# Performance work log

Measured on AMD Instinct MI355X. Metric: run time of the kernel, lower is better.

The kernel has to match this reference:

```python
import jax, jax.numpy as jnp
import numpy as np

B, L, D_IN, D_MODEL, D_OUT, N_LAYERS, N2 = 16, 2048, 512, 512, 512, 4, 32
Q_STEP = 1.0 / 64.0
LN_EPS = 1e-5


def setup_inputs() -> dict:
    key = jax.random.key(0)
    ks = jax.random.split(key, 12)
    H = D_MODEL
    x = jax.random.normal(ks[0], (B, D_IN, L), jnp.float32)
    # sigma-delta dense encoder / decoder weights (ANN-equivalent: dense + ReLU)
    W_enc = jax.random.normal(ks[1], (H, D_IN), jnp.float32) * (1.0 / np.sqrt(D_IN))
    W_dec = jax.random.normal(ks[2], (D_OUT, H), jnp.float32) * (1.0 / np.sqrt(H))
    # S4D kernel params, stacked over layers. S4D-Lin init.
    log_dt = (jax.random.uniform(ks[3], (N_LAYERS, H), jnp.float32)
              * (np.log(0.1) - np.log(0.001)) + np.log(0.001))
    log_A_real = jnp.full((N_LAYERS, H, N2), np.log(0.5), jnp.float32)
    A_imag = jnp.tile((np.pi * jnp.arange(N2, dtype=jnp.float32))[None, None, :],
                      (N_LAYERS, H, 1))
    C_re = jax.random.normal(ks[4], (N_LAYERS, H, N2), jnp.float32) * (0.5 ** 0.5)
    C_im = jax.random.normal(ks[5], (N_LAYERS, H, N2), jnp.float32) * (0.5 ** 0.5)
    D = jax.random.normal(ks[6], (N_LAYERS, H), jnp.float32)
    # output linear of each S4D block: 1x1 conv H -> 2H followed by GLU
    W_out = jax.random.normal(ks[7], (N_LAYERS, 2 * H, H), jnp.float32) * (1.0 / np.sqrt(H))
    b_out = jnp.zeros((N_LAYERS, 2 * H), jnp.float32)
    ln_g = jnp.ones((N_LAYERS, H), jnp.float32)
    ln_b = jnp.zeros((N_LAYERS, H), jnp.float32)
    return {"x": x, "W_enc": W_enc, "W_dec": W_dec, "log_dt": log_dt,
            "log_A_real": log_A_real, "A_imag": A_imag, "C_re": C_re,
            "C_im": C_im, "D": D, "W_out": W_out, "b_out": b_out,
            "ln_g": ln_g, "ln_b": ln_b}


def _quantize_ste(x, step):
    q = jnp.round(x / step) * step
    return x + jax.lax.stop_gradient(q - x)


def reference(x, W_enc, W_dec, log_dt, log_A_real, A_imag, C_re, C_im, D,
              W_out, b_out, ln_g, ln_b):
    # x: (B, d_input, L) channel-time layout (slayer convention)
    xq = _quantize_ste(x, Q_STEP)
    h = jax.nn.relu(jnp.einsum('bct,dc->bdt', xq, W_enc))  # encoder (B,H,L)
    Lx = h.shape[-1]
    t = jnp.arange(Lx)
    for i in range(N_LAYERS):
        # ---- S4D kernel (ZOH-style discretization) ----
        dt = jnp.exp(log_dt[i])[:, None]                 # (H,1)
        A = -jnp.exp(log_A_real[i]) + 1j * A_imag[i]     # (H,N)
        dtA = dt * A                                     # (H,N)
        Cc = (C_re[i] + 1j * C_im[i]) * jnp.expm1(dtA) / A
        vand = jnp.exp(dtA[:, :, None] * t)              # (H,N,L)
        K = 2.0 * jnp.einsum('hn,hnl->hl', Cc, vand).real  # (H,L)
        # ---- FFT convolution ----
        k_f = jnp.fft.rfft(K, n=2 * Lx)                  # (H, L+1)
        u_f = jnp.fft.rfft(h, n=2 * Lx)                  # (B,H,L+1)
        y = jnp.fft.irfft(u_f * k_f[None], n=2 * Lx)[..., :Lx]
        y = y + D[i][:, None] * h                        # skip connection
        y = jax.nn.gelu(y, approximate=False)
        # output linear: 1x1 conv H->2H + GLU over channel dim
        z = jnp.einsum('bht,dh->bdt', y, W_out[i]) + b_out[i][None, :, None]
        z = z[:, :D_MODEL] * jax.nn.sigmoid(z[:, D_MODEL:])
        # residual + post-norm (LayerNorm over channel dim)
        h = z + h
        mu = h.mean(axis=1, keepdims=True)
        var = h.var(axis=1, keepdims=True)
        h = (h - mu) / jnp.sqrt(var + LN_EPS) * ln_g[i][:, None] + ln_b[i][:, None]
    out = jax.nn.relu(jnp.einsum('bht,dh->bdt', h, W_dec))  # decoder (B,d_out,L)
    return out
```

## Files before the change

### kernel.cpp

```cpp
#include <hip/hip_runtime.h>
#include <cstdint>
#include <cstddef>

typedef __attribute__((ext_vector_type(8))) short short8;
typedef __attribute__((ext_vector_type(8))) _Float16 half8;
typedef __attribute__((ext_vector_type(4))) float floatx4;
typedef __attribute__((ext_vector_type(4))) int intx4;
typedef __attribute__((ext_vector_type(4))) unsigned short ushort4v;

__device__ __forceinline__ unsigned short f2h(float f) {
    union { _Float16 h; unsigned short u; } v;
    v.h = (_Float16)f;
    return v.u;
}
__device__ __forceinline__ float h2f(unsigned short u) {
    union { unsigned short u; _Float16 h; } v;
    v.u = u;
    return (float)v.h;
}
__device__ __forceinline__ float relu_keepnan(float v) {
    return v > 0.f ? v : (v == v ? 0.f : v);
}

__global__ __launch_bounds__(256) void k_cvt(
    const float* __restrict__ src, unsigned short* __restrict__ dst, int n) {
    int i = blockIdx.x * 256 + threadIdx.x;
    if (i < n) dst[i] = f2h(src[i]);
}

__global__ __launch_bounds__(256) void k_precompute(
    const float* __restrict__ ldt, const float* __restrict__ lar,
    const float* __restrict__ aim, const float* __restrict__ cre,
    const float* __restrict__ cim, float4* __restrict__ lwc,
    float2* __restrict__ wt) {
    int idx = blockIdx.x * 256 + threadIdx.x;
    int i = idx >> 14;
    int h = (idx >> 5) & 511;
    int n = idx & 31;
    float dt = expf(ldt[i * 512 + h]);
    float Are = -expf(lar[idx]);
    float Aim = aim[idx];
    float dre = dt * Are, dim = dt * Aim;
    float e = expf(dre);
    float wre = e * cosf(dim);
    float wim = e * sinf(dim);
    float emr = wre - 1.f, emi = wim;
    float inv = 1.f / (Are * Are + Aim * Aim);
    float fr = (emr * Are + emi * Aim) * inv;
    float fi = (emi * Are - emr * Aim) * inv;
    float cr = cre[idx], ci = cim[idx];
    float4 o;
    o.x = wre; o.y = wim;
    o.z = 2.f * (cr * fr - ci * fi);
    o.w = 2.f * (cr * fi + ci * fr);
    int oidx = (i * 32 + n) * 512 + h;
    lwc[oidx] = o;
    float ar = wre, ai = wim;
#pragma unroll
    for (int k = 0; k < 7; ++k) {
        float nr = ar * ar - ai * ai;
        float ni = 2.f * ar * ai;
        ar = nr; ai = ni;
    }
    wt[oidx] = make_float2(ar, ai);
}

__global__ __launch_bounds__(256) void k_quant_transpose(
    const float* __restrict__ x, unsigned short* __restrict__ xq, int b0) {
    __shared__ unsigned short tile[64][65];
    const int bg = b0 + blockIdx.z, bl = blockIdx.z;
    const int c0 = blockIdx.y * 64, t0 = blockIdx.x * 64;
    const int tid = threadIdx.x;
#pragma unroll
    for (int it = 0; it < 16; ++it) {
        int idx = it * 256 + tid;
        int r = idx >> 6, cc = idx & 63;
        float f = x[(size_t)(bg * 512 + c0 + r) * 2048 + t0 + cc];
        float q = rintf(f * 64.f) * 0.015625f;
        tile[r][cc] = f2h(q);
    }
    __syncthreads();
#pragma unroll
    for (int it = 0; it < 16; ++it) {
        int idx = it * 256 + tid;
        int r = idx >> 6, cc = idx & 63;
        xq[(size_t)(bl * 2048 + t0 + r) * 512 + c0 + cc] = tile[cc][r];
    }
}

__global__ __launch_bounds__(64) void k_build_wa(
    const float4* __restrict__ lwc, unsigned short* __restrict__ WA, int layer) {
    __shared__ unsigned short Ws[64 * 136];
    const int h = blockIdx.x, tid = threadIdx.x;
    if (tid < 32) {
        float4 v = lwc[((size_t)layer * 32 + tid) * 512 + h];
        float pr = 1.f, pi = 0.f;
        for (int m = 0; m < 128; ++m) {
            Ws[(2 * tid) * 136 + (127 - m)] = f2h(pr);
            Ws[(2 * tid + 1) * 136 + (127 - m)] = f2h(pi);
            float nr = pr * v.x - pi * v.y;
            float ni = pr * v.y + pi * v.x;
            pr = nr; pi = ni;
        }
    }
    __syncthreads();
#pragma unroll
    for (int it = 0; it < 16; ++it) {
        int idx = it * 64 + tid;
        int r = idx >> 4, c8 = idx & 15;
        *(intx4*)(WA + (size_t)h * 8192 + r * 128 + c8 * 8) =
            *(const intx4*)(Ws + r * 136 + c8 * 8);
    }
}

__global__ __launch_bounds__(256) void k_build_T(
    const float4* __restrict__ lwc, const float* __restrict__ Dp,
    unsigned short* __restrict__ TT, int layer) {
    __shared__ float Kvs[128];
    __shared__ unsigned short Mxs[128 * 64];
    __shared__ float wr_s[32], wi_s[32], cr_s[32], ci_s[32];
    const int h = blockIdx.x, tid = threadIdx.x;
    if (tid < 32) {
        float4 v = lwc[((size_t)layer * 32 + tid) * 512 + h];
        wr_s[tid] = v.x; wi_s[tid] = v.y; cr_s[tid] = v.z; ci_s[tid] = v.w;
    }
    __syncthreads();
    if (tid < 32) {
        const int n = tid;
        float wre = wr_s[n], wim = wi_s[n];
        float ar = cr_s[n], ai = ci_s[n];
        for (int m = 0; m <= 128; ++m) {
            if (m < 128) {
                float s = ar;
#pragma unroll
                for (int d = 16; d >= 1; d >>= 1) s += __shfl_xor(s, d, 64);
                if (n == 0) Kvs[m] = s;
            }
            if (m >= 1) {
                Mxs[(m - 1) * 64 + 2 * n] = f2h(ar);
                Mxs[(m - 1) * 64 + 2 * n + 1] = f2h(-ai);
            }
            float nr = ar * wre - ai * wim;
            float ni = ar * wim + ai * wre;
            ar = nr; ai = ni;
        }
    }
    __syncthreads();
    const float Dh = Dp[layer * 512 + h];
#pragma unroll
    for (int it = 0; it < 12; ++it) {
        int idx = it * 256 + tid;
        int t = idx / 24, c8 = idx % 24;
        short8 pack;
#pragma unroll
        for (int q = 0; q < 8; ++q) {
            int k = c8 * 8 + q;
            unsigned short us;
            if (k < 128) {
                float val = (k <= t) ? (Kvs[t - k] + (k == t ? Dh : 0.f)) : 0.f;
                us = f2h(val);
            } else {
                us = Mxs[t * 64 + (k - 128)];
            }
            pack[q] = (short)us;
        }
        *(short8*)(TT + (size_t)h * 24576 + t * 192 + c8 * 8) = pack;
    }
}

template <int MODE>
__global__ __launch_bounds__(256, 2) void k_gemm(
    const unsigned short* __restrict__ A, const unsigned short* __restrict__ Bm,
    float* __restrict__ of32, unsigned short* __restrict__ o16,
    unsigned short* __restrict__ ut, int J, int b0) {
    __shared__ __align__(16) unsigned short lds[2 * 128 * 72];
    unsigned short* Al = lds;
    unsigned short* Bl = lds + 128 * 72;
    const int tid = threadIdx.x;
    const int m0 = blockIdx.y * 128;
    const int j0 = blockIdx.x * 128;
    const int sub = tid & 7;
    const int row = tid >> 3;
    const unsigned short* Ag = A + (size_t)(m0 + row) * 512 + sub * 8;
    const unsigned short* Bg = Bm + (size_t)(j0 + row) * 512 + sub * 8;
    intx4 ra[4], rb[4];
#pragma unroll
    for (int i = 0; i < 4; ++i) {
        ra[i] = *(const intx4*)(Ag + (size_t)i * 32 * 512);
        rb[i] = *(const intx4*)(Bg + (size_t)i * 32 * 512);
    }
    const int lane = tid & 63;
    const int w = tid >> 6;
    const int wm = w & 1, wn = w >> 1;
    const int l15 = lane & 15, quad = lane >> 4;
    floatx4 acc[4][4] = {};
    for (int kt = 0; kt < 8; ++kt) {
#pragma unroll
        for (int i = 0; i < 4; ++i) {
            *(intx4*)(Al + (row + 32 * i) * 72 + sub * 8) = ra[i];
            *(intx4*)(Bl + (row + 32 * i) * 72 + sub * 8) = rb[i];
        }
        __syncthreads();
        if (kt < 7) {
#pragma unroll
            for (int i = 0; i < 4; ++i) {
                ra[i] = *(const intx4*)(Ag + (size_t)i * 32 * 512 + (kt + 1) * 64);
                rb[i] = *(const intx4*)(Bg + (size_t)i * 32 * 512 + (kt + 1) * 64);
            }
        }
#pragma unroll
        for (int ks = 0; ks < 2; ++ks) {
            half8 af[4], bfr[4];
#pragma unroll
            for (int mt = 0; mt < 4; ++mt)
                af[mt] = *(const half8*)(Al + (wm * 64 + mt * 16 + l15) * 72 + ks * 32 + quad * 8);
#pragma unroll
            for (int nt = 0; nt < 4; ++nt)
                bfr[nt] = *(const half8*)(Bl + (wn * 64 + nt * 16 + l15) * 72 + ks * 32 + quad * 8);
#pragma unroll
            for (int mt = 0; mt < 4; ++mt)
#pragma unroll
                for (int nt = 0; nt < 4; ++nt)
                    acc[mt][nt] = __builtin_amdgcn_mfma_f32_16x16x32_f16(
                        af[mt], bfr[nt], acc[mt][nt], 0, 0, 0);
        }
        __syncthreads();
    }
#pragma unroll
    for (int mt = 0; mt < 4; ++mt) {
#pragma unroll
        for (int nt = 0; nt < 4; ++nt) {
            const int dl = wm * 64 + mt * 16 + quad * 4;
            const int jl = wn * 64 + nt * 16 + l15;
            floatx4 v = acc[mt][nt];
#pragma unroll
            for (int r = 0; r < 4; ++r) v[r] = relu_keepnan(v[r]);
            if (MODE == 0) {
                ushort4v hv;
#pragma unroll
                for (int r = 0; r < 4; ++r) hv[r] = f2h(v[r]);
                *(ushort4v*)(o16 + (size_t)(j0 + jl) * 512 + m0 + dl) = hv;
#pragma unroll
                for (int r = 0; r < 4; ++r) lds[(dl + r) * 136 + jl] = hv[r];
            } else {
                const int j = j0 + jl;
                const int bl = j >> 11, t = j & 2047;
#pragma unroll
                for (int r = 0; r < 4; ++r)
                    of32[((size_t)((b0 + bl) * 512 + m0 + dl + r)) * 2048 + t] = v[r];
            }
        }
    }
    if (MODE == 0) {
        __syncthreads();
        const int drow = tid >> 1, hh = tid & 1;
        const unsigned short* srcp = lds + drow * 136 + hh * 64;
        unsigned short* dstp = ut + (size_t)(m0 + drow) * J + j0 + hh * 64;
#pragma unroll
        for (int q = 0; q < 8; ++q)
            *(intx4*)(dstp + q * 8) = *(const intx4*)(srcp + q * 8);
    }
}

__global__ __launch_bounds__(256, 4) void k_stateA(
    const unsigned short* __restrict__ WA, const unsigned short* __restrict__ ut,
    float* __restrict__ P, int J, int Rtot) {
    __shared__ __align__(16) unsigned short Aw[64 * 72];
    __shared__ __align__(16) unsigned short Bw[128 * 72];
    const int tid = threadIdx.x;
    const int h = blockIdx.y;
    const int r0 = blockIdx.x * 128;
    const int sub = tid & 7, row = tid >> 3;
    const unsigned short* Ag = WA + (size_t)h * 8192 + row * 128 + sub * 8;
    const unsigned short* Bg = ut + (size_t)h * J + (size_t)(r0 + row) * 128 + sub * 8;
    intx4 ra[2], rb[4];
    ra[0] = *(const intx4*)(Ag);
    ra[1] = *(const intx4*)(Ag + 32 * 128);
#pragma unroll
    for (int i = 0; i < 4; ++i) rb[i] = *(const intx4*)(Bg + i * 32 * 128);
    const int lane = tid & 63, w = tid >> 6;
    const int wm = w & 1, wn = w >> 1;
    const int l15 = lane & 15, quad = lane >> 4;
    floatx4 acc[2][4] = {};
    for (int kt = 0; kt < 2; ++kt) {
        *(intx4*)(Aw + row * 72 + sub * 8) = ra[0];
        *(intx4*)(Aw + (row + 32) * 72 + sub * 8) = ra[1];
#pragma unroll
        for (int i = 0; i < 4; ++i)
            *(intx4*)(Bw + (row + 32 * i) * 72 + sub * 8) = rb[i];
        __syncthreads();
        if (kt == 0) {
            ra[0] = *(const intx4*)(Ag + 64);
            ra[1] = *(const intx4*)(Ag + 32 * 128 + 64);
#pragma unroll
            for (int i = 0; i < 4; ++i) rb[i] = *(const intx4*)(Bg + i * 32 * 128 + 64);
        }
#pragma unroll
        for (int ks = 0; ks < 2; ++ks) {
            half8 af[2], bfr[4];
#pragma unroll
            for (int mt = 0; mt < 2; ++mt)
                af[mt] = *(const half8*)(Aw + (wm * 32 + mt * 16 + l15) * 72 + ks * 32 + quad * 8);
#pragma unroll
            for (int nt = 0; nt < 4; ++nt)
                bfr[nt] = *(const half8*)(Bw + (wn * 64 + nt * 16 + l15) * 72 + ks * 32 + quad * 8);
#pragma unroll
            for (int mt = 0; mt < 2; ++mt)
#pragma unroll
                for (int nt = 0; nt < 4; ++nt)
                    acc[mt][nt] = __builtin_amdgcn_mfma_f32_16x16x32_f16(
                        af[mt], bfr[nt], acc[mt][nt], 0, 0, 0);
        }
        __syncthreads();
    }
#pragma unroll
    for (int mt = 0; mt < 2; ++mt)
#pragma unroll
        for (int nt = 0; nt < 4; ++nt)
#pragma unroll
            for (int r = 0; r < 4; ++r)
                P[((size_t)h * 64 + wm * 32 + mt * 16 + quad * 4 + r) * Rtot +
                  r0 + wn * 64 + nt * 16 + l15] = acc[mt][nt][r];
}

__global__ __launch_bounds__(64) void k_comb(
    const float* __restrict__ P, const float2* __restrict__ wt,
    unsigned short* __restrict__ S0, int layer, int Rtot) {
    __shared__ float Ps[64][17];
    __shared__ unsigned short S0s[16][64];
    const int h = blockIdx.x, bl = blockIdx.y;
    const int tid = threadIdx.x;
#pragma unroll
    for (int it = 0; it < 4; ++it) {
        int idx = it * 64 + tid;
        int n2 = idx >> 2, pt = idx & 3;
        float4 v = *(const float4*)(P + ((size_t)h * 64 + n2) * Rtot + bl * 16 + pt * 4);
        Ps[n2][pt * 4 + 0] = v.x; Ps[n2][pt * 4 + 1] = v.y;
        Ps[n2][pt * 4 + 2] = v.z; Ps[n2][pt * 4 + 3] = v.w;
    }
    __syncthreads();
    if (tid < 32) {
        const int n = tid;
        float2 wv = wt[((size_t)layer * 32 + n) * 512 + h];
        float ar = 0.f, ai = 0.f;
        for (int g = 0; g < 16; ++g) {
            S0s[g][2 * n] = f2h(ar);
            S0s[g][2 * n + 1] = f2h(ai);
            float pr = Ps[2 * n][g], pi = Ps[2 * n + 1][g];
            float nr = fmaf(wv.x, ar, fmaf(-wv.y, ai, pr));
            float ni = fmaf(wv.x, ai, fmaf(wv.y, ar, pi));
            ar = nr; ai = ni;
        }
    }
    __syncthreads();
    const int g = tid >> 2, pt = tid & 3;
    unsigned short* dst = S0 + ((size_t)h * Rtot + bl * 16 + g) * 64 + pt * 16;
    *(intx4*)(dst) = *(const intx4*)(&S0s[g][pt * 16]);
    *(intx4*)(dst + 8) = *(const intx4*)(&S0s[g][pt * 16 + 8]);
}

__global__ __launch_bounds__(256, 2) void k_applyB(
    const unsigned short* __restrict__ TT, const unsigned short* __restrict__ ut,
    const unsigned short* __restrict__ S0, unsigned short* __restrict__ vt,
    int J, int Rtot) {
    __shared__ __align__(16) unsigned short lds[2 * 128 * 72];
    unsigned short* Al = lds;
    unsigned short* Bl = lds + 128 * 72;
    const int tid = threadIdx.x;
    const int h = blockIdx.y;
    const int r0 = blockIdx.x * 128;
    const int sub = tid & 7, row = tid >> 3;
    const unsigned short* Ag = TT + (size_t)h * 24576 + row * 192 + sub * 8;
    const unsigned short* Bu = ut + (size_t)h * J + (size_t)(r0 + row) * 128 + sub * 8;
    const unsigned short* Bs = S0 + ((size_t)h * Rtot + r0 + row) * 64 + sub * 8;
    intx4 ra[4], rb[4];
#pragma unroll
    for (int i = 0; i < 4; ++i) {
        ra[i] = *(const intx4*)(Ag + i * 32 * 192);
        rb[i] = *(const intx4*)(Bu + i * 32 * 128);
    }
    const int lane = tid & 63, w = tid >> 6;
    const int wm = w & 1, wn = w >> 1;
    const int l15 = lane & 15, quad = lane >> 4;
    floatx4 acc[4][4] = {};
    for (int kt = 0; kt < 3; ++kt) {
#pragma unroll
        for (int i = 0; i < 4; ++i) {
            *(intx4*)(Al + (row + 32 * i) * 72 + sub * 8) = ra[i];
            *(intx4*)(Bl + (row + 32 * i) * 72 + sub * 8) = rb[i];
        }
        __syncthreads();
        if (kt == 0) {
#pragma unroll
            for (int i = 0; i < 4; ++i) {
                ra[i] = *(const intx4*)(Ag + i * 32 * 192 + 64);
                rb[i] = *(const intx4*)(Bu + i * 32 * 128 + 64);
            }
        } else if (kt == 1) {
#pragma unroll
            for (int i = 0; i < 4; ++i) {
                ra[i] = *(const intx4*)(Ag + i * 32 * 192 + 128);
                rb[i] = *(const intx4*)(Bs + i * 32 * 64);
            }
        }
#pragma unroll
        for (int ks = 0; ks < 2; ++ks) {
            half8 af[4], bfr[4];
#pragma unroll
            for (int mt = 0; mt < 4; ++mt)
                af[mt] = *(const half8*)(Al + (wm * 64 + mt * 16 + l15) * 72 + ks * 32 + quad * 8);
#pragma unroll
            for (int nt = 0; nt < 4; ++nt)
                bfr[nt] = *(const half8*)(Bl + (wn * 64 + nt * 16 + l15) * 72 + ks * 32 + quad * 8);
#pragma unroll
            for (int mt = 0; mt < 4; ++mt)
#pragma unroll
                for (int nt = 0; nt < 4; ++nt)
                    acc[mt][nt] = __builtin_amdgcn_mfma_f32_16x16x32_f16(
                        af[mt], bfr[nt], acc[mt][nt], 0, 0, 0);
        }
        __syncthreads();
    }
#pragma unroll
    for (int mt = 0; mt < 4; ++mt)
#pragma unroll
        for (int nt = 0; nt < 4; ++nt) {
            const int tl = wm * 64 + mt * 16 + quad * 4;
            const int rl = wn * 64 + nt * 16 + l15;
            ushort4v pack;
#pragma unroll
            for (int r = 0; r < 4; ++r) {
                float y = acc[mt][nt][r];
                float ge = 0.5f * y * (1.f + erff(y * 0.70710678118654752f));
                pack[r] = f2h(ge);
            }
            *(ushort4v*)(lds + rl * 136 + tl) = pack;
        }
    __syncthreads();
    const int rl2 = tid >> 1, hh = tid & 1;
    const unsigned short* srcp = lds + rl2 * 136 + hh * 64;
    unsigned short* dstp = vt + (size_t)h * J + (size_t)(r0 + rl2) * 128 + hh * 64;
#pragma unroll
    for (int q = 0; q < 8; ++q)
        *(intx4*)(dstp + q * 8) = *(const intx4*)(srcp + q * 8);
}

__global__ __launch_bounds__(256, 2) void k_gemm_glu(
    const unsigned short* __restrict__ A,
    const unsigned short* __restrict__ Bt,
    const float* __restrict__ bias,
    unsigned short* __restrict__ g_out, int J) {
    __shared__ __align__(16) unsigned short A1l[128 * 72];
    __shared__ __align__(16) unsigned short A2l[128 * 72];
    __shared__ __align__(16) unsigned short Bl[128 * 72];
    const int tid = threadIdx.x;
    const int m0 = blockIdx.y * 128;
    const int j0 = blockIdx.x * 128;
    const int sub = tid & 7;
    const int row = tid >> 3;
    const unsigned short* A1g = A + (size_t)(m0 + row) * 512 + sub * 8;
    const unsigned short* A2g = A1g + 512 * 512;
    const int chp = tid >> 3, jo = tid & 7;
    const unsigned short* Bg = Bt + (size_t)(2 * chp) * J + j0 + jo * 8;
    intx4 ra1[4], ra2[4], rb[4];
#pragma unroll
    for (int i = 0; i < 4; ++i) {
        ra1[i] = *(const intx4*)(A1g + (size_t)i * 32 * 512);
        ra2[i] = *(const intx4*)(A2g + (size_t)i * 32 * 512);
    }
    rb[0] = *(const intx4*)(Bg);
    rb[1] = *(const intx4*)(Bg + J);
    rb[2] = *(const intx4*)(Bg + 64);
    rb[3] = *(const intx4*)(Bg + J + 64);
    const int lane = tid & 63;
    const int w = tid >> 6;
    const int wm = w & 1, wn = w >> 1;
    const int l15 = lane & 15, quad = lane >> 4;
    const int colbase = (((chp >> 2) ^ jo) << 3) + (chp & 3) * 2;
    floatx4 ac1[4][4] = {}, ac2[4][4] = {};
    for (int kt = 0; kt < 8; ++kt) {
#pragma unroll
        for (int i = 0; i < 4; ++i) {
            *(intx4*)(A1l + (row + 32 * i) * 72 + sub * 8) = ra1[i];
            *(intx4*)(A2l + (row + 32 * i) * 72 + sub * 8) = ra2[i];
        }
        {
            unsigned int* B32 = (unsigned int*)Bl;
#pragma unroll
            for (int half = 0; half < 2; ++half) {
                const int jb = (jo + half * 8) * 8;
                intx4 e0 = rb[half * 2], e1 = rb[half * 2 + 1];
#pragma unroll
                for (int i = 0; i < 4; ++i) {
                    unsigned int ae = (unsigned int)e0[i], be = (unsigned int)e1[i];
                    unsigned int lo = (ae & 0xffffu) | (be << 16);
                    unsigned int hi = (ae >> 16) | (be & 0xffff0000u);
                    B32[((jb + 2 * i) * 72 + colbase) >> 1] = lo;
                    B32[((jb + 2 * i + 1) * 72 + colbase) >> 1] = hi;
                }
            }
        }
        __syncthreads();
        if (kt < 7) {
#pragma unroll
            for (int i = 0; i < 4; ++i) {
                ra1[i] = *(const intx4*)(A1g + (size_t)i * 32 * 512 + (kt + 1) * 64);
                ra2[i] = *(const intx4*)(A2g + (size_t)i * 32 * 512 + (kt + 1) * 64);
            }
            rb[0] = *(const intx4*)(Bg + (size_t)(kt + 1) * 64 * J);
            rb[1] = *(const intx4*)(Bg + (size_t)(kt + 1) * 64 * J + J);
            rb[2] = *(const intx4*)(Bg + (size_t)(kt + 1) * 64 * J + 64);
            rb[3] = *(const intx4*)(Bg + (size_t)(kt + 1) * 64 * J + J + 64);
        }
#pragma unroll
        for (int ks = 0; ks < 2; ++ks) {
            half8 af1[4], af2[4], bfr[4];
#pragma unroll
            for (int mt = 0; mt < 4; ++mt) {
                af1[mt] = *(const half8*)(A1l + (wm * 64 + mt * 16 + l15) * 72 + ks * 32 + quad * 8);
                af2[mt] = *(const half8*)(A2l + (wm * 64 + mt * 16 + l15) * 72 + ks * 32 + quad * 8);
            }
#pragma unroll
            for (int nt = 0; nt < 4; ++nt) {
                const int rr = wn * 64 + nt * 16 + l15;
                const int cb = (ks * 4 + quad) ^ ((rr >> 3) & 7);
                bfr[nt] = *(const half8*)(Bl + rr * 72 + cb * 8);
            }
#pragma unroll
            for (int mt = 0; mt < 4; ++mt)
#pragma unroll
                for (int nt = 0; nt < 4; ++nt) {
                    ac1[mt][nt] = __builtin_amdgcn_mfma_f32_16x16x32_f16(
                        af1[mt], bfr[nt], ac1[mt][nt], 0, 0, 0);
                    ac2[mt][nt] = __builtin_amdgcn_mfma_f32_16x16x32_f16(
                        af2[mt], bfr[nt], ac2[mt][nt], 0, 0, 0);
                }
        }
        __syncthreads();
    }
#pragma unroll
    for (int mt = 0; mt < 4; ++mt) {
#pragma unroll
        for (int nt = 0; nt < 4; ++nt) {
            const int d = m0 + wm * 64 + mt * 16 + quad * 4;
            const int j = j0 + wn * 64 + nt * 16 + l15;
            ushort4v v;
#pragma unroll
            for (int r = 0; r < 4; ++r) {
                float a = ac1[mt][nt][r] + bias[d + r];
                float gg = ac2[mt][nt][r] + bias[512 + d + r];
                v[r] = f2h(a / (1.f + expf(-gg)));
            }
            *(ushort4v*)(g_out + (size_t)j * 512 + d) = v;
        }
    }
}

__global__ __launch_bounds__(256, 4) void k_res_ln_t(
    const unsigned short* __restrict__ g, unsigned short* __restrict__ hf,
    unsigned short* __restrict__ ut, unsigned short* __restrict__ hb,
    const float* __restrict__ lng, const float* __restrict__ lnb,
    int layer, int J, int mode) {
    __shared__ unsigned short tile[64 * 40];
    const int tid = threadIdx.x;
    const int r = tid >> 3, sub = tid & 7;
    const int j0 = blockIdx.x * 32;
    const size_t j = (size_t)j0 + r;
    const unsigned short* gj = g + j * 512;
    unsigned short* hj = hf + j * 512;
    floatx4 v[16];
    float s1 = 0.f, s2 = 0.f;
#pragma unroll
    for (int k = 0; k < 16; ++k) {
        ushort4v gv = *(const ushort4v*)(gj + sub * 4 + k * 32);
        ushort4v hv = *(const ushort4v*)(hj + sub * 4 + k * 32);
        floatx4 vv;
#pragma unroll
        for (int i = 0; i < 4; ++i) vv[i] = h2f(gv[i]) + h2f(hv[i]);
        v[k] = vv;
        s1 += vv[0] + vv[1] + vv[2] + vv[3];
        s2 += vv[0] * vv[0] + vv[1] * vv[1] + vv[2] * vv[2] + vv[3] * vv[3];
    }
#pragma unroll
    for (int m = 4; m >= 1; m >>= 1) { s1 += __shfl_xor(s1, m, 64); s2 += __shfl_xor(s2, m, 64); }
    const float mu = s1 * (1.f / 512.f);
    const float var = s2 * (1.f / 512.f) - mu * mu;
    const float isd = 1.f / sqrtf(var + 1e-5f);
#pragma unroll
    for (int t = 0; t < 8; ++t) {
        if (mode == 1 && t) __syncthreads();
#pragma unroll
        for (int kk = 0; kk < 2; ++kk) {
            const int k = t * 2 + kk;
            const int cho = sub * 4 + k * 32;
            floatx4 gw = *(const floatx4*)(lng + layer * 512 + cho);
            floatx4 bw = *(const floatx4*)(lnb + layer * 512 + cho);
            ushort4v p;
#pragma unroll
            for (int i = 0; i < 4; ++i)
                p[i] = f2h((v[k][i] - mu) * isd * gw[i] + bw[i]);
            if (mode == 1) {
                *(ushort4v*)(hj + cho) = p;
                const int chl = kk * 32 + sub * 4;
#pragma unroll
                for (int i = 0; i < 4; ++i)
                    tile[(chl + i) * 40 + (r ^ ((((chl + i) >> 2) & 3) << 3))] = p[i];
            } else {
                *(ushort4v*)(hb + j * 512 + cho) = p;
            }
        }
        if (mode == 1) {
            __syncthreads();
            const int chrow = tid >> 2, part = tid & 3;
            const int pb = part ^ ((chrow >> 2) & 3);
            *(intx4*)(ut + (size_t)(t * 64 + chrow) * J + j0 + part * 8) =
                *(const intx4*)(tile + chrow * 40 + pb * 8);
        }
    }
}

extern "C" void kernel_launch(void* const* d_in, const int* in_sizes, int n_in,
                              void* d_out, int out_size, void* d_ws, size_t ws_size,
                              hipStream_t stream) {
    (void)in_sizes; (void)n_in; (void)out_size;
    const float* x      = (const float*)d_in[0];
    const float* W_enc  = (const float*)d_in[1];
    const float* W_dec  = (const float*)d_in[2];
    const float* log_dt = (const float*)d_in[3];
    const float* log_Ar = (const float*)d_in[4];
    const float* A_im   = (const float*)d_in[5];
    const float* C_re   = (const float*)d_in[6];
    const float* C_im   = (const float*)d_in[7];
    const float* Dp     = (const float*)d_in[8];
    const float* W_out  = (const float*)d_in[9];
    const float* b_out  = (const float*)d_in[10];
    const float* ln_g   = (const float*)d_in[11];
    const float* ln_b   = (const float*)d_in[12];

    int C = 16;
    while (C > 8 && (size_t)C * (9ull << 20) + (42ull << 20) > ws_size) C >>= 1;
    const size_t J = (size_t)C * 2048;
    const int Rtot = C * 16;

    char* ws = (char*)d_ws;
    size_t off = 0;
    auto alloc = [&](size_t bytes) { void* p = ws + off; off += (bytes + 255) & ~(size_t)255; return p; };
    float4*         lwc   = (float4*)alloc(4ull * 512 * 32 * 16);
    float2*         wt    = (float2*)alloc(4ull * 512 * 32 * 8);
    unsigned short* wencb = (unsigned short*)alloc(512 * 512 * 2);
    unsigned short* wdecb = (unsigned short*)alloc(512 * 512 * 2);
    unsigned short* woutb = (unsigned short*)alloc(4ull * 1024 * 512 * 2);
    unsigned short* WAb   = (unsigned short*)alloc(512ull * 64 * 128 * 2);
    unsigned short* TTb   = (unsigned short*)alloc(512ull * 128 * 192 * 2);
    unsigned short* ut    = (unsigned short*)alloc(512ull * J * 2);
    char*           scan  = (char*)alloc((size_t)C * (3ull << 20));
    unsigned short* hf    = (unsigned short*)alloc(J * 512 * 2);
    unsigned short* vt    = (unsigned short*)alloc(J * 512 * 2);
    unsigned short* g16   = (unsigned short*)scan;
    unsigned short* xq    = (unsigned short*)scan;
    unsigned short* hb    = vt;
    float*          P     = (float*)scan;
    unsigned short* S0u   = (unsigned short*)(scan + (size_t)C * (2ull << 20));

    k_precompute<<<256, 256, 0, stream>>>(log_dt, log_Ar, A_im, C_re, C_im, lwc, wt);
    k_cvt<<<1024, 256, 0, stream>>>(W_enc, wencb, 512 * 512);
    k_cvt<<<1024, 256, 0, stream>>>(W_dec, wdecb, 512 * 512);
    k_cvt<<<8192, 256, 0, stream>>>(W_out, woutb, 4 * 1024 * 512);
    for (int b0 = 0; b0 < 16; b0 += C) {
        k_quant_transpose<<<dim3(32, 8, C), 256, 0, stream>>>(x, xq, b0);
        k_gemm<0><<<dim3(C * 16, 4), 256, 0, stream>>>(wencb, xq, nullptr, hf, ut, (int)J, 0);
        for (int i = 0; i < 4; ++i) {
            k_build_wa<<<512, 64, 0, stream>>>(lwc, WAb, i);
            k_build_T<<<512, 256, 0, stream>>>(lwc, Dp, TTb, i);
            k_stateA<<<dim3(Rtot / 128, 512), 256, 0, stream>>>(WAb, ut, P, (int)J, Rtot);
            k_comb<<<dim3(512, C), 64, 0, stream>>>(P, wt, S0u, i, Rtot);
            k_applyB<<<dim3(Rtot / 128, 512), 256, 0, stream>>>(TTb, ut, S0u, vt, (int)J, Rtot);
            k_gemm_glu<<<dim3(C * 16, 4), 256, 0, stream>>>(
                woutb + (size_t)i * 1024 * 512, vt, b_out + (size_t)i * 1024, g16, (int)J);
            k_res_ln_t<<<(int)(J / 32), 256, 0, stream>>>(
                g16, hf, ut, hb, ln_g, ln_b, i, (int)J, (i == 3) ? 2 : 1);
        }
        k_gemm<2><<<dim3(C * 16, 4), 256, 0, stream>>>(wdecb, hb, (float*)d_out, nullptr, nullptr, (int)J, b0);
    }
}
```

Before: 1.022 ms.

## Load GLU GEMM A fragments from global, double-buffer B, stage output via LDS

The GLU GEMM kernel no longer stages the weight tiles (A1/A2) through shared memory. Each wave now reads its MFMA A fragments straight from global memory, relying on cache since the weights are small and shared across blocks. The B tile is double-buffered in LDS, which removes the second barrier in each k-iteration. The epilogue writes results to LDS and then emits coalesced 16-byte row stores, replacing the scattered 8-byte stores. The cost is global-load latency on the MFMA critical path and more L2/L1 traffic per wave.

```diff
diff --git a/kernel.cpp b/kernel.cpp
--- a/kernel.cpp
+++ b/kernel.cpp
@@ -450,42 +450,28 @@
     const unsigned short* __restrict__ Bt,
     const float* __restrict__ bias,
     unsigned short* __restrict__ g_out, int J) {
-    __shared__ __align__(16) unsigned short A1l[128 * 72];
-    __shared__ __align__(16) unsigned short A2l[128 * 72];
-    __shared__ __align__(16) unsigned short Bl[128 * 72];
+    __shared__ __align__(16) unsigned short Bl[2 * 128 * 72];
     const int tid = threadIdx.x;
     const int m0 = blockIdx.y * 128;
     const int j0 = blockIdx.x * 128;
-    const int sub = tid & 7;
-    const int row = tid >> 3;
-    const unsigned short* A1g = A + (size_t)(m0 + row) * 512 + sub * 8;
-    const unsigned short* A2g = A1g + 512 * 512;
     const int chp = tid >> 3, jo = tid & 7;
     const unsigned short* Bg = Bt + (size_t)(2 * chp) * J + j0 + jo * 8;
-    intx4 ra1[4], ra2[4], rb[4];
-#pragma unroll
-    for (int i = 0; i < 4; ++i) {
-        ra1[i] = *(const intx4*)(A1g + (size_t)i * 32 * 512);
-        ra2[i] = *(const intx4*)(A2g + (size_t)i * 32 * 512);
-    }
+    const int lane = tid & 63;
+    const int w = tid >> 6;
+    const int wm = w & 1, wn = w >> 1;
+    const int l15 = lane & 15, quad = lane >> 4;
+    const unsigned short* A1f = A + (size_t)(m0 + wm * 64 + l15) * 512 + quad * 8;
+    const unsigned short* A2f = A1f + 512 * 512;
+    intx4 rb[4];
     rb[0] = *(const intx4*)(Bg);
     rb[1] = *(const intx4*)(Bg + J);
     rb[2] = *(const intx4*)(Bg + 64);
     rb[3] = *(const intx4*)(Bg + J + 64);
-    const int lane = tid & 63;
-    const int w = tid >> 6;
-    const int wm = w & 1, wn = w >> 1;
-    const int l15 = lane & 15, quad = lane >> 4;
     const int colbase = (((chp >> 2) ^ jo) << 3) + (chp & 3) * 2;
     floatx4 ac1[4][4] = {}, ac2[4][4] = {};
     for (int kt = 0; kt < 8; ++kt) {
-#pragma unroll
-        for (int i = 0; i < 4; ++i) {
-            *(intx4*)(A1l + (row + 32 * i) * 72 + sub * 8) = ra1[i];
-            *(intx4*)(A2l + (row + 32 * i) * 72 + sub * 8) = ra2[i];
-        }
         {
-            unsigned int* B32 = (unsigned int*)Bl;
+            unsigned int* B32 = (unsigned int*)(Bl + (kt & 1) * 9216);
 #pragma unroll
             for (int half = 0; half < 2; ++half) {
                 const int jb = (jo + half * 8) * 8;
@@ -502,29 +488,25 @@
         }
         __syncthreads();
         if (kt < 7) {
-#pragma unroll
-            for (int i = 0; i < 4; ++i) {
-                ra1[i] = *(const intx4*)(A1g + (size_t)i * 32 * 512 + (kt + 1) * 64);
-                ra2[i] = *(const intx4*)(A2g + (size_t)i * 32 * 512 + (kt + 1) * 64);
-            }
             rb[0] = *(const intx4*)(Bg + (size_t)(kt + 1) * 64 * J);
             rb[1] = *(const intx4*)(Bg + (size_t)(kt + 1) * 64 * J + J);
             rb[2] = *(const intx4*)(Bg + (size_t)(kt + 1) * 64 * J + 64);
             rb[3] = *(const intx4*)(Bg + (size_t)(kt + 1) * 64 * J + J + 64);
         }
+        const unsigned short* Bcur = Bl + (kt & 1) * 9216;
 #pragma unroll
         for (int ks = 0; ks < 2; ++ks) {
             half8 af1[4], af2[4], bfr[4];
 #pragma unroll
             for (int mt = 0; mt < 4; ++mt) {
-                af1[mt] = *(const half8*)(A1l + (wm * 64 + mt * 16 + l15) * 72 + ks * 32 + quad * 8);
-                af2[mt] = *(const half8*)(A2l + (wm * 64 + mt * 16 + l15) * 72 + ks * 32 + quad * 8);
+                af1[mt] = *(const half8*)(A1f + (size_t)mt * 16 * 512 + kt * 64 + ks * 32);
+                af2[mt] = *(const half8*)(A2f + (size_t)mt * 16 * 512 + kt * 64 + ks * 32);
             }
 #pragma unroll
             for (int nt = 0; nt < 4; ++nt) {
                 const int rr = wn * 64 + nt * 16 + l15;
                 const int cb = (ks * 4 + quad) ^ ((rr >> 3) & 7);
-                bfr[nt] = *(const half8*)(Bl + rr * 72 + cb * 8);
+                bfr[nt] = *(const half8*)(Bcur + rr * 72 + cb * 8);
             }
 #pragma unroll
             for (int mt = 0; mt < 4; ++mt)
@@ -536,24 +518,31 @@
                         af2[mt], bfr[nt], ac2[mt][nt], 0, 0, 0);
                 }
         }
-        __syncthreads();
-    }
+    }
+    __syncthreads();
 #pragma unroll
     for (int mt = 0; mt < 4; ++mt) {
 #pragma unroll
         for (int nt = 0; nt < 4; ++nt) {
-            const int d = m0 + wm * 64 + mt * 16 + quad * 4;
-            const int j = j0 + wn * 64 + nt * 16 + l15;
-            ushort4v v;
+            const int dl = wm * 64 + mt * 16 + quad * 4;
+            const int jl = wn * 64 + nt * 16 + l15;
+            ushort4v p;
 #pragma unroll
             for (int r = 0; r < 4; ++r) {
-                float a = ac1[mt][nt][r] + bias[d + r];
-                float gg = ac2[mt][nt][r] + bias[512 + d + r];
-                v[r] = f2h(a / (1.f + expf(-gg)));
-            }
-            *(ushort4v*)(g_out + (size_t)j * 512 + d) = v;
-        }
-    }
+                float a = ac1[mt][nt][r] + bias[m0 + dl + r];
+                float gg = ac2[mt][nt][r] + bias[512 + m0 + dl + r];
+                p[r] = f2h(a / (1.f + expf(-gg)));
+            }
+            *(ushort4v*)(Bl + jl * 136 + dl) = p;
+        }
+    }
+    __syncthreads();
+    const int r2 = tid >> 1, hh = tid & 1;
+    const unsigned short* srcp = Bl + r2 * 136 + hh * 64;
+    unsigned short* dstp = g_out + (size_t)(j0 + r2) * 512 + m0 + hh * 64;
+#pragma unroll
+    for (int q = 0; q < 8; ++q)
+        *(intx4*)(dstp + q * 8) = *(const intx4*)(srcp + q * 8);
 }
 
 __global__ __launch_bounds__(256, 4) void k_res_ln_t(
```

Measured after the change: 1.187 ms. 16.1% more time.
